# Performance work log

Measured on AMD Instinct MI355X. Metric: run time of the kernel, lower is better.

## Reference

```python
import jax, jax.numpy as jnp
import numpy as np

K_NEIGHBORS = 32  # n_neighbors, eval mode -> displacement = 0


def setup_inputs() -> dict:
    key = jax.random.key(0)
    ks = jax.random.split(key, 9)
    B, N, F = 1024, 200000, 64
    C, H = 16, 128
    return {
        "x": jax.random.normal(ks[0], (B, F), jnp.float32),
        "X_data": jax.random.normal(ks[1], (N, F), jnp.float32),
        "y": jax.random.uniform(ks[2], (N,), jnp.float32),
        "W_gate": jax.random.normal(ks[3], (F + 1, C), jnp.float32) / np.sqrt(F + 1),
        "b_gate": jax.random.normal(ks[4], (C,), jnp.float32) * 0.01,
        "W1": jax.random.normal(ks[5], (C + F, H), jnp.float32) / np.sqrt(C + F),
        "b1": jax.random.normal(ks[6], (H,), jnp.float32) * 0.01,
        "W_last": jax.random.normal(ks[7], (H, 1), jnp.float32) / np.sqrt(H),
        "b_last": jax.random.normal(ks[8], (1,), jnp.float32) * 0.01,
    }


def reference(x, X_data, y, W_gate, b_gate, W1, b1, W_last, b_last):
    # Euclidean (p=2) cdist via the expanded form: ||a-b||^2 = ||a||^2 + ||b||^2 - 2 a.b
    d2 = (jnp.sum(x * x, axis=1, keepdims=True)
          + jnp.sum(X_data * X_data, axis=1)[None, :]
          - 2.0 * (x @ X_data.T))                      # [B, N]
    dist = jnp.sqrt(jnp.maximum(d2, 0.0))
    # torch.argsort(distances,1)[:, :k] == indices of k smallest distances
    _, idx = jax.lax.top_k(-dist, K_NEIGHBORS)          # [B, K]
    neighbors = X_data[idx]                             # [B, K, F] gather
    neighbors_y = y[idx][..., None]                     # [B, K, 1]
    nf = jnp.concatenate([neighbors, neighbors_y], axis=2)  # [B, K, F+1]
    gated = jnp.tanh(nf @ W_gate + b_gate)              # [B, K, C]
    agg = jnp.sum(gated, axis=1)                        # [B, C]
    o = jnp.concatenate([x, agg], axis=1)               # [B, F+C]
    o = jnp.tanh(o @ W1 + b1)                           # activation_function = tanh
    o = jax.nn.sigmoid(o @ W_last + b_last)             # [B, 1]
    return o
```

## Files before the change

kernel.cpp:

```cpp
#include <hip/hip_runtime.h>
#include <cstdint>

#define FDIM 64
#define KNN 32
#define NBUCKET 256
#define MAXCAP 2048
#define SEG 10
#define OCAP 512

typedef unsigned int u32;
typedef unsigned long long u64;
typedef __attribute__((ext_vector_type(8))) short bf16x8;
typedef __attribute__((ext_vector_type(4))) float f32x4;

__device__ __forceinline__ float load_query(const float* __restrict__ x, int q, float4* xv) {
    const float4* xp = (const float4*)(x + (size_t)q * FDIM);
    float n0 = 0.f, n1 = 0.f, n2 = 0.f, n3 = 0.f;
#pragma unroll
    for (int k = 0; k < 16; ++k) {
        float4 v = xp[k];
        xv[k] = v;
        n0 = fmaf(v.x, v.x, n0); n1 = fmaf(v.y, v.y, n1);
        n2 = fmaf(v.z, v.z, n2); n3 = fmaf(v.w, v.w, n3);
    }
    return (n0 + n1) + (n2 + n3);
}

__device__ __forceinline__ float dot_row(const float4* __restrict__ xv, const float* __restrict__ row) {
    const float4* rv = (const float4*)row;
    float d0 = 0.f, d1 = 0.f, d2 = 0.f, d3 = 0.f;
#pragma unroll
    for (int k = 0; k < 16; ++k) {
        float4 r = rv[k];
        float4 a = xv[k];
        d0 = fmaf(a.x, r.x, d0); d1 = fmaf(a.y, r.y, d1);
        d2 = fmaf(a.z, r.z, d2); d3 = fmaf(a.w, r.w, d3);
    }
    return (d0 + d1) + (d2 + d3);
}

__global__ __launch_bounds__(256) void k_xnorm(const float* __restrict__ X, float* __restrict__ Xn, int N) {
    int i = blockIdx.x * 256 + threadIdx.x;
    if (i >= N) return;
    const float4* r = (const float4*)(X + (size_t)i * FDIM);
    float d0 = 0.f, d1 = 0.f, d2 = 0.f, d3 = 0.f;
#pragma unroll
    for (int k = 0; k < 16; ++k) {
        float4 v = r[k];
        d0 = fmaf(v.x, v.x, d0); d1 = fmaf(v.y, v.y, d1);
        d2 = fmaf(v.z, v.z, d2); d3 = fmaf(v.w, v.w, d3);
    }
    Xn[i] = (d0 + d1) + (d2 + d3);
}

__global__ __launch_bounds__(256) void k_cvtT(const float* __restrict__ src, uint4* __restrict__ dst, int n_u4) {
    int i = blockIdx.x * 256 + threadIdx.x;
    if (i >= n_u4) return;
    int lane = i & 63;
    int kk = (i >> 6) & 1;
    int g = i >> 7;
    int row = g * 16 + (lane & 15);
    int col = kk * 32 + (lane >> 4) * 8;
    const float4* s = (const float4*)(src + (size_t)row * FDIM + col);
    float4 a = s[0], b = s[1];
    ushort o[8];
    const float* f = &a.x;
#pragma unroll
    for (int k = 0; k < 4; ++k) {
        u32 u = __float_as_uint(f[k]);
        o[k] = (ushort)((u + 0x7fffu + ((u >> 16) & 1u)) >> 16);
    }
    const float* gg = &b.x;
#pragma unroll
    for (int k = 0; k < 4; ++k) {
        u32 u = __float_as_uint(gg[k]);
        o[4 + k] = (ushort)((u + 0x7fffu + ((u >> 16) & 1u)) >> 16);
    }
    dst[i] = *(uint4*)o;
}

__global__ __launch_bounds__(256) void k_hist(const float* __restrict__ x, const float* __restrict__ X,
                                              const float* __restrict__ Xn, u32* __restrict__ hist,
                                              int N, int nsamp, int sj) {
    __shared__ unsigned char h8[NBUCKET * 256];
    int t = threadIdx.x;
    u32* h32 = (u32*)h8;
#pragma unroll
    for (int k = 0; k < 64; ++k) h32[k * 256 + t] = 0;
    __syncthreads();
    int q = blockIdx.x * 256 + t;
    float4 xv[16];
    float xn = load_query(x, q, xv);
    for (int j = 0; j < sj; ++j) {
        int s = blockIdx.y * sj + j;
        int p = s * 16;
        if (s < nsamp && p < N) {
            float dp = dot_row(xv, X + (size_t)p * FDIM);
            float d2 = fmaxf(xn + Xn[p] - 2.f * dp, 0.f);
            int b = min(NBUCKET - 1, (int)d2);
            int idx = b * 256 + t;
            unsigned char v = h8[idx];
            h8[idx] = (v == 255u) ? v : (unsigned char)(v + 1);
        }
    }
    __syncthreads();
#pragma unroll
    for (int w = 0; w < 128; ++w) {
        u32 v0 = h8[(2 * w) * 256 + t];
        u32 v1 = h8[(2 * w + 1) * 256 + t];
        if (v0 | v1) atomicAdd(&hist[(size_t)q * 128 + w], v0 | (v1 << 16));
    }
}

__global__ __launch_bounds__(256) void k_thresh(const u32* __restrict__ hist, float* __restrict__ Tq, int B) {
    int q = blockIdx.x * 256 + threadIdx.x;
    if (q >= B) return;
    const u32* h = hist + (size_t)q * 128;
    int cum = 0;
    float T = (float)NBUCKET;
    for (int w = 0; w < 128; ++w) {
        u32 v = h[w];
        cum += (int)(v & 0xffffu);
        if (cum >= KNN) { T = (float)(2 * w + 1); break; }
        cum += (int)(v >> 16);
        if (cum >= KNN) { T = (float)(2 * w + 2); break; }
    }
    Tq[q] = T + 2.0f;
}

__global__ __launch_bounds__(256, 3) void k_sample_d2(
        const uint4* __restrict__ xT, const uint4* __restrict__ XT,
        const float* __restrict__ qn, const float* __restrict__ Xn,
        unsigned char* __restrict__ d2s, int S) {
    int t = threadIdx.x;
    int w = t >> 6, lane = t & 63;
    int G = lane >> 4, r = lane & 15;
    int qg = blockIdx.x;
    int wq = qg * 128 + w * 32;
    int pb = blockIdx.y * 128;

    bf16x8 afr[2][2];
#pragma unroll
    for (int kk = 0; kk < 2; ++kk)
#pragma unroll
        for (int mi = 0; mi < 2; ++mi) {
            uint4 v = xT[(size_t)(((wq >> 4) + mi) * 2 + kk) * 64 + lane];
            afr[kk][mi] = *(bf16x8*)&v;
        }
    float qr[8];
#pragma unroll
    for (int e = 0; e < 8; ++e)
        qr[e] = qn[wq + (e >> 2) * 16 + G * 4 + (e & 3)];

#pragma unroll
    for (int half = 0; half < 2; ++half) {
        int nb = half * 4;
        bf16x8 bfr[4][2];
#pragma unroll
        for (int j = 0; j < 4; ++j) {
            int gp = (pb >> 4) + nb + j;
#pragma unroll
            for (int kk = 0; kk < 2; ++kk) {
                uint4 v = XT[(size_t)(gp * 2 + kk) * 64 + lane];
                bfr[j][kk] = *(bf16x8*)&v;
            }
        }
        float xnv[4];
#pragma unroll
        for (int j = 0; j < 4; ++j) xnv[j] = Xn[pb + (nb + j) * 16 + r];

        f32x4 acc[2][4];
#pragma unroll
        for (int mi = 0; mi < 2; ++mi)
#pragma unroll
            for (int j = 0; j < 4; ++j) acc[mi][j] = (f32x4){0.f, 0.f, 0.f, 0.f};
#pragma unroll
        for (int kk = 0; kk < 2; ++kk)
#pragma unroll
            for (int j = 0; j < 4; ++j) {
                acc[0][j] = __builtin_amdgcn_mfma_f32_16x16x32_bf16(afr[kk][0], bfr[j][kk], acc[0][j], 0, 0, 0);
                acc[1][j] = __builtin_amdgcn_mfma_f32_16x16x32_bf16(afr[kk][1], bfr[j][kk], acc[1][j], 0, 0, 0);
            }
#pragma unroll
        for (int j = 0; j < 4; ++j) {
            int p = pb + (nb + j) * 16 + r;
            float xnp = xnv[j];
#pragma unroll
            for (int e = 0; e < 8; ++e) {
                float d2a = qr[e] + fmaf(-2.f, acc[e >> 2][j][e & 3], xnp);
                int b = (int)d2a;
                b = b < 0 ? 0 : (b > 255 ? 255 : b);
                int q = wq + (e >> 2) * 16 + G * 4 + (e & 3);
                d2s[(size_t)q * S + p] = (unsigned char)b;
            }
        }
    }
}

__global__ __launch_bounds__(256) void k_thresh2(const unsigned char* __restrict__ d2s,
                                                 float* __restrict__ Tq, int S) {
    __shared__ u32 h[NBUCKET];
    int t = threadIdx.x;
    int q = blockIdx.x;
    h[t] = 0;
    __syncthreads();
    const u32* row = (const u32*)(d2s + (size_t)q * S);
    int n4 = S >> 2;
    for (int i = t; i < n4; i += 256) {
        u32 v = row[i];
        atomicAdd(&h[v & 255u], 1u);
        atomicAdd(&h[(v >> 8) & 255u], 1u);
        atomicAdd(&h[(v >> 16) & 255u], 1u);
        atomicAdd(&h[v >> 24], 1u);
    }
    __syncthreads();
    if (t == 0) {
        int cum = 0;
        float T = 256.0f;
        for (int b = 0; b < NBUCKET; ++b) {
            cum += (int)h[b];
            if (cum >= KNN) { T = (float)(b + 1); break; }
        }
        Tq[q] = T + 2.0f;
    }
}

__global__ __launch_bounds__(256, 3) void k_mfma_filter(
        const uint4* __restrict__ xT, const uint4* __restrict__ XT,
        const float* __restrict__ qn, const float* __restrict__ Xn,
        const float* __restrict__ Tf,
        u32* __restrict__ cnt_seg, u32* __restrict__ list_seg,
        u32* __restrict__ ocnt, u32* __restrict__ olist,
        int N, int nStripsPad, int strip) {
    __shared__ u32 ldsCnt[128];

    int t = threadIdx.x;
    int w = t >> 6, lane = t & 63;
    int G = lane >> 4, r = lane & 15;

    int bid = blockIdx.x;
    int qg = (bid >> 3) & 7;
    int sIdx = (bid & 7) | ((bid >> 6) << 3);
    int qbase = qg * 128;
    int wq = qbase + w * 32;

    if (t < 128) ldsCnt[t] = 0;
    __syncthreads();

    bf16x8 afr[2][2];
#pragma unroll
    for (int kk = 0; kk < 2; ++kk)
#pragma unroll
        for (int mi = 0; mi < 2; ++mi) {
            uint4 v = xT[(size_t)(((wq >> 4) + mi) * 2 + kk) * 64 + lane];
            afr[kk][mi] = *(bf16x8*)&v;
        }
    float Tr[8];
#pragma unroll
    for (int e = 0; e < 8; ++e) {
        int rl = wq + (e >> 2) * 16 + G * 4 + (e & 3);
        Tr[e] = Tf[rl] - qn[rl];
    }

    u32* segBase = list_seg + ((size_t)qbase * nStripsPad + (size_t)sIdx) * SEG;

    for (int s = 0; s < strip; ++s) {
        int pb = (sIdx * strip + s) * 128;
        if (pb >= N) break;

#pragma unroll
        for (int half = 0; half < 2; ++half) {
            int nb = half * 4;
            bf16x8 bfr[4][2];
#pragma unroll
            for (int j = 0; j < 4; ++j) {
                int gp = (pb >> 4) + nb + j;
#pragma unroll
                for (int kk = 0; kk < 2; ++kk) {
                    uint4 v = XT[(size_t)(gp * 2 + kk) * 64 + lane];
                    bfr[j][kk] = *(bf16x8*)&v;
                }
            }
            float xnv[4];
#pragma unroll
            for (int j = 0; j < 4; ++j) xnv[j] = Xn[pb + (nb + j) * 16 + r];

            f32x4 acc[2][4];
#pragma unroll
            for (int mi = 0; mi < 2; ++mi)
#pragma unroll
                for (int j = 0; j < 4; ++j) acc[mi][j] = (f32x4){0.f, 0.f, 0.f, 0.f};
#pragma unroll
            for (int kk = 0; kk < 2; ++kk)
#pragma unroll
                for (int j = 0; j < 4; ++j) {
                    acc[0][j] = __builtin_amdgcn_mfma_f32_16x16x32_bf16(afr[kk][0], bfr[j][kk], acc[0][j], 0, 0, 0);
                    acc[1][j] = __builtin_amdgcn_mfma_f32_16x16x32_bf16(afr[kk][1], bfr[j][kk], acc[1][j], 0, 0, 0);
                }
#pragma unroll
            for (int j = 0; j < 4; ++j) {
                int p = pb + (nb + j) * 16 + r;
                float xnp = xnv[j];
                bool c0 = fmaf(-2.f, acc[0][j][0], xnp) < Tr[0];
                bool c1 = fmaf(-2.f, acc[0][j][1], xnp) < Tr[1];
                bool c2 = fmaf(-2.f, acc[0][j][2], xnp) < Tr[2];
                bool c3 = fmaf(-2.f, acc[0][j][3], xnp) < Tr[3];
                bool c4 = fmaf(-2.f, acc[1][j][0], xnp) < Tr[4];
                bool c5 = fmaf(-2.f, acc[1][j][1], xnp) < Tr[5];
                bool c6 = fmaf(-2.f, acc[1][j][2], xnp) < Tr[6];
                bool c7 = fmaf(-2.f, acc[1][j][3], xnp) < Tr[7];
                if ((c0 | c1 | c2 | c3 | c4 | c5 | c6 | c7) && p < N) {
#pragma unroll
                    for (int e = 0; e < 8; ++e) {
                        bool ce = (e == 0) ? c0 : (e == 1) ? c1 : (e == 2) ? c2 : (e == 3) ? c3
                                : (e == 4) ? c4 : (e == 5) ? c5 : (e == 6) ? c6 : c7;
                        if (ce) {
                            int ql = w * 32 + (e >> 2) * 16 + G * 4 + (e & 3);
                            u32 slot = atomicAdd(&ldsCnt[ql], 1u);
                            if (slot < SEG) {
                                segBase[(size_t)ql * nStripsPad * SEG + slot] = (u32)p;
                            } else {
                                u32 gs = atomicAdd(&ocnt[qbase + ql], 1u);
                                if (gs < OCAP) olist[(size_t)(qbase + ql) * OCAP + gs] = (u32)p;
                            }
                        }
                    }
                }
            }
        }
    }

    __syncthreads();
    if (t < 128) cnt_seg[(size_t)(qbase + t) * nStripsPad + sIdx] = min(ldsCnt[t], (u32)SEG);
}

__global__ __launch_bounds__(256) void k_filter_scalar(const float* __restrict__ x, const float* __restrict__ X,
                                                       const float* __restrict__ Xn, const float* __restrict__ Tq,
                                                       u32* __restrict__ cnt, u32* __restrict__ list,
                                                       int N, int cap) {
    int t = threadIdx.x;
    int q = blockIdx.x * 256 + t;
    float4 xv[16];
    float xn = load_query(x, q, xv);
    float T = Tq[q];
    int base = blockIdx.y * 1024;
    int lim = min(1024, N - base);
    for (int j = 0; j < lim; ++j) {
        int p = base + j;
        float dp = dot_row(xv, X + (size_t)p * FDIM);
        float d2 = fmaxf(xn + Xn[p] - 2.f * dp, 0.f);
        if (d2 < T) {
            u32 slot = atomicAdd(&cnt[q], 1u);
            if (slot < (u32)cap) list[(size_t)q * cap + slot] = (u32)p;
        }
    }
}

__global__ __launch_bounds__(256) void k_final(const float* __restrict__ x, const float* __restrict__ X,
                                               const float* __restrict__ y, const float* __restrict__ Xn,
                                               const float* __restrict__ Wg, const float* __restrict__ bg,
                                               const float* __restrict__ W1, const float* __restrict__ b1,
                                               const float* __restrict__ Wl, const float* __restrict__ bl,
                                               const u32* __restrict__ cnt_seg, const u32* __restrict__ list_seg,
                                               const u32* __restrict__ ocnt, const u32* __restrict__ olist,
                                               const u32* __restrict__ cnt_flat, const u32* __restrict__ list_flat,
                                               float* __restrict__ out, int nStripsPad, int cap_flat, int flat,
                                               int N) {
    __shared__ u64 keys[MAXCAP];
    __shared__ u32 nsh;
    __shared__ u64 wk[4];
    __shared__ int wp[4];
    __shared__ u32 sel[KNN];
    __shared__ float gkc[KNN * 16];
    __shared__ float aggc[16];
    __shared__ float red[128];

    int t = threadIdx.x;
    int w = t >> 6, lane = t & 63;
    int q = blockIdx.x;
    int m;

    if (flat) {
        m = (int)min(cnt_flat[q], (u32)cap_flat);
        const u32* lq = list_flat + (size_t)q * cap_flat;
        for (int i = t; i < m; i += 256) keys[i] = lq[i];
    } else {
        if (t == 0) nsh = 0;
        __syncthreads();
        for (int seg = t; seg < nStripsPad; seg += 256) {
            u32 c = cnt_seg[(size_t)q * nStripsPad + seg];
            if (c) {
                u32 base = atomicAdd(&nsh, c);
                const u32* sp = list_seg + ((size_t)q * nStripsPad + seg) * SEG;
                for (u32 j = 0; j < c; ++j) {
                    u32 idx = base + j;
                    if (idx < MAXCAP) keys[idx] = sp[j];
                }
            }
        }
        __syncthreads();
        int m0 = (int)min(nsh, (u32)MAXCAP);
        int oc = (int)min(ocnt[q], (u32)OCAP);
        for (int i = t; i < oc; i += 256)
            if (m0 + i < MAXCAP) keys[m0 + i] = olist[(size_t)q * OCAP + i];
        m = min(m0 + oc, MAXCAP);
    }
    __syncthreads();

    {
        int ch = lane & 15;
        int rsub = lane >> 4;
        float4 xq4 = ((const float4*)(x + (size_t)q * FDIM))[ch];
        float xs = fmaf(xq4.x, xq4.x, fmaf(xq4.y, xq4.y, fmaf(xq4.z, xq4.z, xq4.w * xq4.w)));
        xs += __shfl_xor(xs, 1);
        xs += __shfl_xor(xs, 2);
        xs += __shfl_xor(xs, 4);
        xs += __shfl_xor(xs, 8);
        float xn = xs;
        for (int base = w * 32; base < m; base += 128) {
            int ri[8]; u32 pp[8]; bool val[8]; float4 vv[8];
#pragma unroll
            for (int u = 0; u < 8; ++u) {
                ri[u] = base + u * 4 + rsub;
                val[u] = ri[u] < m;
                pp[u] = val[u] ? (u32)keys[ri[u]] : 0u;
            }
#pragma unroll
            for (int u = 0; u < 8; ++u)
                vv[u] = ((const float4*)(X + (size_t)pp[u] * FDIM))[ch];
#pragma unroll
            for (int u = 0; u < 8; ++u) {
                float part = fmaf(xq4.x, vv[u].x, fmaf(xq4.y, vv[u].y, fmaf(xq4.z, vv[u].z, xq4.w * vv[u].w)));
                part += __shfl_xor(part, 1);
                part += __shfl_xor(part, 2);
                part += __shfl_xor(part, 4);
                part += __shfl_xor(part, 8);
                if (val[u] && ch == 0) {
                    float d2 = fmaxf(xn + Xn[pp[u]] - 2.f * part, 0.f);
                    keys[ri[u]] = ((u64)__float_as_uint(d2) << 32) | pp[u];
                }
            }
        }
    }
    __syncthreads();

    if (m <= 512) {
        if (w == 0) {
            u64 rk[8];
#pragma unroll
            for (int i = 0; i < 8; ++i) {
                int idx = lane + (i << 6);
                rk[i] = (idx < m) ? keys[idx] : ~0ull;
            }
            for (int r = 0; r < KNN; ++r) {
                u64 bk = ~0ull;
                int bs = 0;
#pragma unroll
                for (int i = 0; i < 8; ++i)
                    if (rk[i] < bk) { bk = rk[i]; bs = i; }
                int bo = lane;
#pragma unroll
                for (int off = 1; off < 64; off <<= 1) {
                    u64 ok = __shfl_xor(bk, off);
                    int oo = __shfl_xor(bo, off);
                    if (ok < bk) { bk = ok; bo = oo; }
                }
                if (lane == bo) rk[bs] = ~0ull;
                if (lane == 0) sel[r] = (u32)bk;
            }
        }
        __syncthreads();
    } else {
        for (int r = 0; r < KNN; ++r) {
            u64 bk = ~0ull;
            int bp = -1;
            for (int i = t; i < m; i += 256) {
                u64 k = keys[i];
                if (k < bk) { bk = k; bp = i; }
            }
#pragma unroll
            for (int off = 32; off > 0; off >>= 1) {
                u64 ok = __shfl_down(bk, off);
                int op = __shfl_down(bp, off);
                if (ok < bk) { bk = ok; bp = op; }
            }
            if (lane == 0) { wk[w] = bk; wp[w] = bp; }
            __syncthreads();
            if (t == 0) {
                u64 fb = wk[0];
                int fp = wp[0];
                for (int v = 1; v < 4; ++v)
                    if (wk[v] < fb) { fb = wk[v]; fp = wp[v]; }
                sel[r] = (u32)(fb & 0xffffffffu);
                if (fp >= 0) keys[fp] = ~0ull;
            }
            __syncthreads();
        }
    }

    int c = t & 15, kk = t >> 4;
#pragma unroll
    for (int rep = 0; rep < 2; ++rep) {
        int k = kk + 16 * rep;
        int nb = min((int)sel[k], N - 1);
        const float* Xr = X + (size_t)nb * FDIM;
        float acc = bg[c];
#pragma unroll
        for (int f = 0; f < FDIM; ++f) acc = fmaf(Xr[f], Wg[f * 16 + c], acc);
        acc = fmaf(y[nb], Wg[FDIM * 16 + c], acc);
        gkc[k * 16 + c] = tanhf(acc);
    }
    __syncthreads();
    if (t < 16) {
        float s = 0.f;
#pragma unroll
        for (int k = 0; k < KNN; ++k) s += gkc[k * 16 + t];
        aggc[t] = s;
    }
    __syncthreads();
    if (t < 128) {
        const float* xq = x + (size_t)q * FDIM;
        float acc = b1[t];
#pragma unroll
        for (int f = 0; f < FDIM; ++f) acc = fmaf(xq[f], W1[f * 128 + t], acc);
#pragma unroll
        for (int cc2 = 0; cc2 < 16; ++cc2) acc = fmaf(aggc[cc2], W1[(FDIM + cc2) * 128 + t], acc);
        red[t] = tanhf(acc) * Wl[t];
    }
    __syncthreads();
    for (int off = 64; off > 0; off >>= 1) {
        if (t < off) red[t] += red[t + off];
        __syncthreads();
    }
    if (t == 0) out[q] = 1.f / (1.f + expf(-(red[0] + bl[0])));
}

extern "C" void kernel_launch(void* const* d_in, const int* in_sizes, int n_in,
                              void* d_out, int out_size, void* d_ws, size_t ws_size,
                              hipStream_t stream) {
    const float* x  = (const float*)d_in[0];
    const float* X  = (const float*)d_in[1];
    const float* y  = (const float*)d_in[2];
    const float* Wg = (const float*)d_in[3];
    const float* bg = (const float*)d_in[4];
    const float* W1 = (const float*)d_in[5];
    const float* b1 = (const float*)d_in[6];
    const float* Wl = (const float*)d_in[7];
    const float* bl = (const float*)d_in[8];
    float* out = (float*)d_out;

    int B = in_sizes[0] / FDIM;
    int N = in_sizes[1] / FDIM;

    const int strip = 8;
    int nTiles = (N + 127) / 128;
    int nStrips = (nTiles + strip - 1) / strip;
    nStrips = (nStrips + 7) & ~7;
    int nStripsPad = nStrips;
    int Npad = nStrips * strip * 128;

    char* w = (char*)d_ws;
    size_t off = 0;
    auto alloc = [&](size_t bytes) { void* p = w + off; off += (bytes + 255) & ~(size_t)255; return p; };
    float* Xn  = (float*)alloc((size_t)Npad * 4);
    float* qn  = (float*)alloc((size_t)B * 4);
    u32* hist  = (u32*)alloc((size_t)B * 512);
    float* Tq  = (float*)alloc((size_t)B * 4);
    u32* cnt   = (u32*)alloc((size_t)B * 4);

    size_t xTB = (size_t)B * 128;
    size_t XTB = (size_t)(Npad / 16) * 2048;
    size_t segCntB = (size_t)B * nStripsPad * 4;
    size_t segListB = (size_t)B * nStripsPad * SEG * 4;
    size_t ocntB = (size_t)B * 4;
    size_t olistB = (size_t)B * OCAP * 4;
    size_t rem = (ws_size > off) ? ws_size - off : 0;
    bool mfma_path = rem >= xTB + XTB + segCntB + segListB + ocntB + olistB + 4096;

    uint4* xT = nullptr; uint4* XT = nullptr;
    u32 *cnt_seg = nullptr, *list_seg = nullptr, *ocnt = nullptr, *olist = nullptr;
    u32* list_flat = nullptr; unsigned char* d2s = nullptr;
    int cap_flat = 64, Stiles = 0;
    if (mfma_path) {
        xT = (uint4*)alloc(xTB);
        XT = (uint4*)alloc(XTB);
        cnt_seg  = (u32*)alloc(segCntB);
        list_seg = (u32*)alloc(segListB);
        ocnt     = (u32*)alloc(ocntB);
        olist    = (u32*)alloc(olistB);
        rem = (ws_size > off) ? ws_size - off : 0;
        size_t st = rem / ((size_t)B * 128);
        Stiles = st > 198 ? 198 : (int)st;
        int maxFull = N / 128;
        if (Stiles > maxFull) Stiles = maxFull;
        if (Stiles >= 96) d2s = (unsigned char*)alloc((size_t)Stiles * 128 * B);
        else Stiles = 0;
    } else {
        size_t c = rem / ((size_t)B * 4);
        cap_flat = c > MAXCAP ? MAXCAP : (int)c;
        if (cap_flat < 64) cap_flat = 64;
        list_flat = (u32*)alloc((size_t)B * cap_flat * 4);
    }

    k_xnorm<<<dim3((N + 255) / 256), 256, 0, stream>>>(X, Xn, N);
    k_xnorm<<<dim3((B + 255) / 256), 256, 0, stream>>>(x, qn, B);

    if (mfma_path) {
        hipMemsetAsync(ocnt, 0, ocntB, stream);
        hipMemsetAsync(Xn + N, 0, (size_t)(Npad - N) * 4, stream);
        size_t realXT = (size_t)(N / 16) * 2048;
        hipMemsetAsync((char*)XT + realXT, 0, XTB - realXT, stream);

        int nxu4 = B * 8, nXu4 = N * 8;
        k_cvtT<<<dim3((nxu4 + 255) / 256), 256, 0, stream>>>(x, xT, nxu4);
        k_cvtT<<<dim3((nXu4 + 255) / 256), 256, 0, stream>>>(X, XT, nXu4);

        if (Stiles > 0) {
            int S = Stiles * 128;
            k_sample_d2<<<dim3(8, Stiles), 256, 0, stream>>>(xT, XT, qn, Xn, d2s, S);
            k_thresh2<<<dim3(B), 256, 0, stream>>>(d2s, Tq, S);
        } else {
            hipMemsetAsync(hist, 0, (size_t)B * 512, stream);
            int nsamp = (N + 15) / 16;
            int chunks = 128;
            int sj = (nsamp + chunks - 1) / chunks;
            k_hist<<<dim3(B / 256, chunks), 256, 0, stream>>>(x, X, Xn, hist, N, nsamp, sj);
            k_thresh<<<dim3((B + 255) / 256), 256, 0, stream>>>(hist, Tq, B);
        }

        k_mfma_filter<<<dim3(8 * nStrips), 256, 0, stream>>>(
            xT, XT, qn, Xn, Tq, cnt_seg, list_seg, ocnt, olist, N, nStripsPad, strip);

        k_final<<<dim3(B), 256, 0, stream>>>(x, X, y, Xn, Wg, bg, W1, b1, Wl, bl,
                                             cnt_seg, list_seg, ocnt, olist,
                                             nullptr, nullptr, out, nStripsPad, 0, 0, N);
    } else {
        hipMemsetAsync(cnt, 0, (size_t)B * 4, stream);
        hipMemsetAsync(hist, 0, (size_t)B * 512, stream);
        int nsamp = (N + 15) / 16;
        int chunks = 128;
        int sj = (nsamp + chunks - 1) / chunks;
        k_hist<<<dim3(B / 256, chunks), 256, 0, stream>>>(x, X, Xn, hist, N, nsamp, sj);
        k_thresh<<<dim3((B + 255) / 256), 256, 0, stream>>>(hist, Tq, B);
        k_filter_scalar<<<dim3(B / 256, (N + 1023) / 1024), 256, 0, stream>>>(
            x, X, Xn, Tq, cnt, list_flat, N, cap_flat);
        k_final<<<dim3(B), 256, 0, stream>>>(x, X, y, Xn, Wg, bg, W1, b1, Wl, bl,
                                             nullptr, nullptr, nullptr, nullptr,
                                             cnt, list_flat, out, nStripsPad, cap_flat, 1, N);
    }
}
```

Measured before the change: 287.4 us.

## Split final kernel into gather, parallel rescore, and select stages

```diff
diff --git a/kernel.cpp b/kernel.cpp
--- a/kernel.cpp
+++ b/kernel.cpp
@@ -356,18 +356,89 @@
     }
 }
 
-__global__ __launch_bounds__(256) void k_final(const float* __restrict__ x, const float* __restrict__ X,
-                                               const float* __restrict__ y, const float* __restrict__ Xn,
-                                               const float* __restrict__ Wg, const float* __restrict__ bg,
-                                               const float* __restrict__ W1, const float* __restrict__ b1,
-                                               const float* __restrict__ Wl, const float* __restrict__ bl,
-                                               const u32* __restrict__ cnt_seg, const u32* __restrict__ list_seg,
-                                               const u32* __restrict__ ocnt, const u32* __restrict__ olist,
-                                               const u32* __restrict__ cnt_flat, const u32* __restrict__ list_flat,
-                                               float* __restrict__ out, int nStripsPad, int cap_flat, int flat,
-                                               int N) {
+__global__ __launch_bounds__(256) void k_gather(const u32* __restrict__ cnt_seg, const u32* __restrict__ list_seg,
+                                                const u32* __restrict__ ocnt, const u32* __restrict__ olist,
+                                                u64* __restrict__ gkeys, u32* __restrict__ gcnt,
+                                                int nStripsPad) {
+    __shared__ u32 nsh;
+    int t = threadIdx.x;
+    int q = blockIdx.x;
+    if (t == 0) nsh = 0;
+    __syncthreads();
+    u64* gq = gkeys + (size_t)q * MAXCAP;
+    for (int seg = t; seg < nStripsPad; seg += 256) {
+        u32 c = cnt_seg[(size_t)q * nStripsPad + seg];
+        if (c) {
+            u32 base = atomicAdd(&nsh, c);
+            const u32* sp = list_seg + ((size_t)q * nStripsPad + seg) * SEG;
+            for (u32 j = 0; j < c; ++j) {
+                u32 idx = base + j;
+                if (idx < MAXCAP) gq[idx] = (u64)sp[j];
+            }
+        }
+    }
+    __syncthreads();
+    u32 m0 = min(nsh, (u32)MAXCAP);
+    u32 oc = min(ocnt[q], (u32)OCAP);
+    for (u32 i = t; i < oc; i += 256)
+        if (m0 + i < MAXCAP) gq[m0 + i] = (u64)olist[(size_t)q * OCAP + i];
+    if (t == 0) gcnt[q] = min(m0 + oc, (u32)MAXCAP);
+}
+
+__global__ __launch_bounds__(256, 4) void k_rescore(const float* __restrict__ x, const float* __restrict__ X,
+                                                    const float* __restrict__ Xn,
+                                                    u64* __restrict__ gkeys, const u32* __restrict__ gcnt) {
+    int t = threadIdx.x;
+    int w = t >> 6, lane = t & 63;
+    int q = blockIdx.x;
+    int g = blockIdx.y;
+    int m = (int)gcnt[q];
+    u64* gq = gkeys + (size_t)q * MAXCAP;
+
+    int ch = lane & 15;
+    int rsub = lane >> 4;
+    float4 xq4 = ((const float4*)(x + (size_t)q * FDIM))[ch];
+    float xs = fmaf(xq4.x, xq4.x, fmaf(xq4.y, xq4.y, fmaf(xq4.z, xq4.z, xq4.w * xq4.w)));
+    xs += __shfl_xor(xs, 1);
+    xs += __shfl_xor(xs, 2);
+    xs += __shfl_xor(xs, 4);
+    xs += __shfl_xor(xs, 8);
+    float xn = xs;
+
+    for (int base = (g * 4 + w) * 32; base < m; base += 256) {
+        int ri[8]; u32 pp[8]; bool val[8]; float4 vv[8];
+#pragma unroll
+        for (int u = 0; u < 8; ++u) {
+            ri[u] = base + u * 4 + rsub;
+            val[u] = ri[u] < m;
+            pp[u] = val[u] ? (u32)gq[ri[u]] : 0u;
+        }
+#pragma unroll
+        for (int u = 0; u < 8; ++u)
+            vv[u] = ((const float4*)(X + (size_t)pp[u] * FDIM))[ch];
+#pragma unroll
+        for (int u = 0; u < 8; ++u) {
+            float part = fmaf(xq4.x, vv[u].x, fmaf(xq4.y, vv[u].y, fmaf(xq4.z, vv[u].z, xq4.w * vv[u].w)));
+            part += __shfl_xor(part, 1);
+            part += __shfl_xor(part, 2);
+            part += __shfl_xor(part, 4);
+            part += __shfl_xor(part, 8);
+            if (val[u] && ch == 0) {
+                float d2 = fmaxf(xn + Xn[pp[u]] - 2.f * part, 0.f);
+                gq[ri[u]] = ((u64)__float_as_uint(d2) << 32) | pp[u];
+            }
+        }
+    }
+}
+
+__global__ __launch_bounds__(256) void k_select_nn(const float* __restrict__ x, const float* __restrict__ X,
+                                                   const float* __restrict__ y,
+                                                   const float* __restrict__ Wg, const float* __restrict__ bg,
+                                                   const float* __restrict__ W1, const float* __restrict__ b1,
+                                                   const float* __restrict__ Wl, const float* __restrict__ bl,
+                                                   const u64* __restrict__ gkeys, const u32* __restrict__ gcnt,
+                                                   float* __restrict__ out, int N) {
     __shared__ u64 keys[MAXCAP];
-    __shared__ u32 nsh;
     __shared__ u64 wk[4];
     __shared__ int wp[4];
     __shared__ u32 sel[KNN];
@@ -378,70 +449,10 @@
     int t = threadIdx.x;
     int w = t >> 6, lane = t & 63;
     int q = blockIdx.x;
-    int m;
-
-    if (flat) {
-        m = (int)min(cnt_flat[q], (u32)cap_flat);
-        const u32* lq = list_flat + (size_t)q * cap_flat;
-        for (int i = t; i < m; i += 256) keys[i] = lq[i];
-    } else {
-        if (t == 0) nsh = 0;
-        __syncthreads();
-        for (int seg = t; seg < nStripsPad; seg += 256) {
-            u32 c = cnt_seg[(size_t)q * nStripsPad + seg];
-            if (c) {
-                u32 base = atomicAdd(&nsh, c);
-                const u32* sp = list_seg + ((size_t)q * nStripsPad + seg) * SEG;
-                for (u32 j = 0; j < c; ++j) {
-                    u32 idx = base + j;
-                    if (idx < MAXCAP) keys[idx] = sp[j];
-                }
-            }
-        }
-        __syncthreads();
-        int m0 = (int)min(nsh, (u32)MAXCAP);
-        int oc = (int)min(ocnt[q], (u32)OCAP);
-        for (int i = t; i < oc; i += 256)
-            if (m0 + i < MAXCAP) keys[m0 + i] = olist[(size_t)q * OCAP + i];
-        m = min(m0 + oc, MAXCAP);
-    }
-    __syncthreads();
-
-    {
-        int ch = lane & 15;
-        int rsub = lane >> 4;
-        float4 xq4 = ((const float4*)(x + (size_t)q * FDIM))[ch];
-        float xs = fmaf(xq4.x, xq4.x, fmaf(xq4.y, xq4.y, fmaf(xq4.z, xq4.z, xq4.w * xq4.w)));
-        xs += __shfl_xor(xs, 1);
-        xs += __shfl_xor(xs, 2);
-        xs += __shfl_xor(xs, 4);
-        xs += __shfl_xor(xs, 8);
-        float xn = xs;
-        for (int base = w * 32; base < m; base += 128) {
-            int ri[8]; u32 pp[8]; bool val[8]; float4 vv[8];
-#pragma unroll
-            for (int u = 0; u < 8; ++u) {
-                ri[u] = base + u * 4 + rsub;
-                val[u] = ri[u] < m;
-                pp[u] = val[u] ? (u32)keys[ri[u]] : 0u;
-            }
-#pragma unroll
-            for (int u = 0; u < 8; ++u)
-                vv[u] = ((const float4*)(X + (size_t)pp[u] * FDIM))[ch];
-#pragma unroll
-            for (int u = 0; u < 8; ++u) {
-                float part = fmaf(xq4.x, vv[u].x, fmaf(xq4.y, vv[u].y, fmaf(xq4.z, vv[u].z, xq4.w * vv[u].w)));
-                part += __shfl_xor(part, 1);
-                part += __shfl_xor(part, 2);
-                part += __shfl_xor(part, 4);
-                part += __shfl_xor(part, 8);
-                if (val[u] && ch == 0) {
-                    float d2 = fmaxf(xn + Xn[pp[u]] - 2.f * part, 0.f);
-                    keys[ri[u]] = ((u64)__float_as_uint(d2) << 32) | pp[u];
-                }
-            }
-        }
-    }
+    int m = (int)gcnt[q];
+    const u64* gq = gkeys + (size_t)q * MAXCAP;
+
+    for (int i = t; i < m; i += 256) keys[i] = gq[i];
     __syncthreads();
 
     if (m <= 512) {
@@ -496,6 +507,102 @@
             }
             __syncthreads();
         }
+    }
+
+    int c = t & 15, kk = t >> 4;
+#pragma unroll
+    for (int rep = 0; rep < 2; ++rep) {
+        int k = kk + 16 * rep;
+        int nb = min((int)sel[k], N - 1);
+        const float* Xr = X + (size_t)nb * FDIM;
+        float acc = bg[c];
+#pragma unroll
+        for (int f = 0; f < FDIM; ++f) acc = fmaf(Xr[f], Wg[f * 16 + c], acc);
+        acc = fmaf(y[nb], Wg[FDIM * 16 + c], acc);
+        gkc[k * 16 + c] = tanhf(acc);
+    }
+    __syncthreads();
+    if (t < 16) {
+        float s = 0.f;
+#pragma unroll
+        for (int k = 0; k < KNN; ++k) s += gkc[k * 16 + t];
+        aggc[t] = s;
+    }
+    __syncthreads();
+    if (t < 128) {
+        const float* xq = x + (size_t)q * FDIM;
+        float acc = b1[t];
+#pragma unroll
+        for (int f = 0; f < FDIM; ++f) acc = fmaf(xq[f], W1[f * 128 + t], acc);
+#pragma unroll
+        for (int cc2 = 0; cc2 < 16; ++cc2) acc = fmaf(aggc[cc2], W1[(FDIM + cc2) * 128 + t], acc);
+        red[t] = tanhf(acc) * Wl[t];
+    }
+    __syncthreads();
+    for (int off = 64; off > 0; off >>= 1) {
+        if (t < off) red[t] += red[t + off];
+        __syncthreads();
+    }
+    if (t == 0) out[q] = 1.f / (1.f + expf(-(red[0] + bl[0])));
+}
+
+__global__ __launch_bounds__(256) void k_final_flat(const float* __restrict__ x, const float* __restrict__ X,
+                                                    const float* __restrict__ y, const float* __restrict__ Xn,
+                                                    const float* __restrict__ Wg, const float* __restrict__ bg,
+                                                    const float* __restrict__ W1, const float* __restrict__ b1,
+                                                    const float* __restrict__ Wl, const float* __restrict__ bl,
+                                                    const u32* __restrict__ cnt_flat, const u32* __restrict__ list_flat,
+                                                    float* __restrict__ out, int cap_flat, int N) {
+    __shared__ u64 keys[MAXCAP];
+    __shared__ u64 wk[4];
+    __shared__ int wp[4];
+    __shared__ u32 sel[KNN];
+    __shared__ float gkc[KNN * 16];
+    __shared__ float aggc[16];
+    __shared__ float red[128];
+
+    int t = threadIdx.x;
+    int w = t >> 6, lane = t & 63;
+    int q = blockIdx.x;
+    int m = (int)min(cnt_flat[q], (u32)cap_flat);
+    const u32* lq = list_flat + (size_t)q * cap_flat;
+    for (int i = t; i < m; i += 256) keys[i] = lq[i];
+    __syncthreads();
+
+    float4 xv[16];
+    float xn = load_query(x, q, xv);
+    for (int i = t; i < m; i += 256) {
+        u32 p = (u32)keys[i];
+        float dp = dot_row(xv, X + (size_t)p * FDIM);
+        float d2 = fmaxf(xn + Xn[p] - 2.f * dp, 0.f);
+        keys[i] = ((u64)__float_as_uint(d2) << 32) | p;
+    }
+    __syncthreads();
+
+    for (int r = 0; r < KNN; ++r) {
+        u64 bk = ~0ull;
+        int bp = -1;
+        for (int i = t; i < m; i += 256) {
+            u64 k = keys[i];
+            if (k < bk) { bk = k; bp = i; }
+        }
+#pragma unroll
+        for (int off = 32; off > 0; off >>= 1) {
+            u64 ok = __shfl_down(bk, off);
+            int op = __shfl_down(bp, off);
+            if (ok < bk) { bk = ok; bp = op; }
+        }
+        if (lane == 0) { wk[w] = bk; wp[w] = bp; }
+        __syncthreads();
+        if (t == 0) {
+            u64 fb = wk[0];
+            int fp = wp[0];
+            for (int v = 1; v < 4; ++v)
+                if (wk[v] < fb) { fb = wk[v]; fp = wp[v]; }
+            sel[r] = (u32)(fb & 0xffffffffu);
+            if (fp >= 0) keys[fp] = ~0ull;
+        }
+        __syncthreads();
     }
 
     int c = t & 15, kk = t >> 4;
@@ -574,11 +681,14 @@
     size_t segListB = (size_t)B * nStripsPad * SEG * 4;
     size_t ocntB = (size_t)B * 4;
     size_t olistB = (size_t)B * OCAP * 4;
+    size_t gkeysB = (size_t)B * MAXCAP * 8;
+    size_t gcntB = (size_t)B * 4;
     size_t rem = (ws_size > off) ? ws_size - off : 0;
-    bool mfma_path = rem >= xTB + XTB + segCntB + segListB + ocntB + olistB + 4096;
+    bool mfma_path = rem >= xTB + XTB + segCntB + segListB + ocntB + olistB + gkeysB + gcntB + 4096;
 
     uint4* xT = nullptr; uint4* XT = nullptr;
     u32 *cnt_seg = nullptr, *list_seg = nullptr, *ocnt = nullptr, *olist = nullptr;
+    u64* gkeys = nullptr; u32* gcnt = nullptr;
     u32* list_flat = nullptr; unsigned char* d2s = nullptr;
     int cap_flat = 64, Stiles = 0;
     if (mfma_path) {
@@ -588,6 +698,8 @@
         list_seg = (u32*)alloc(segListB);
         ocnt     = (u32*)alloc(ocntB);
         olist    = (u32*)alloc(olistB);
+        gkeys    = (u64*)alloc(gkeysB);
+        gcnt     = (u32*)alloc(gcntB);
         rem = (ws_size > off) ? ws_size - off : 0;
         size_t st = rem / ((size_t)B * 128);
         Stiles = st > 198 ? 198 : (int)st;
@@ -631,9 +743,10 @@
         k_mfma_filter<<<dim3(8 * nStrips), 256, 0, stream>>>(
             xT, XT, qn, Xn, Tq, cnt_seg, list_seg, ocnt, olist, N, nStripsPad, strip);
 
-        k_final<<<dim3(B), 256, 0, stream>>>(x, X, y, Xn, Wg, bg, W1, b1, Wl, bl,
-                                             cnt_seg, list_seg, ocnt, olist,
-                                             nullptr, nullptr, out, nStripsPad, 0, 0, N);
+        k_gather<<<dim3(B), 256, 0, stream>>>(cnt_seg, list_seg, ocnt, olist, gkeys, gcnt, nStripsPad);
+        k_rescore<<<dim3(B, 2), 256, 0, stream>>>(x, X, Xn, gkeys, gcnt);
+        k_select_nn<<<dim3(B), 256, 0, stream>>>(x, X, y, Wg, bg, W1, b1, Wl, bl,
+                                                 gkeys, gcnt, out, N);
     } else {
         hipMemsetAsync(cnt, 0, (size_t)B * 4, stream);
         hipMemsetAsync(hist, 0, (size_t)B * 512, stream);
@@ -644,8 +757,7 @@
         k_thresh<<<dim3((B + 255) / 256), 256, 0, stream>>>(hist, Tq, B);
         k_filter_scalar<<<dim3(B / 256, (N + 1023) / 1024), 256, 0, stream>>>(
             x, X, Xn, Tq, cnt, list_flat, N, cap_flat);
-        k_final<<<dim3(B), 256, 0, stream>>>(x, X, y, Xn, Wg, bg, W1, b1, Wl, bl,
-                                             nullptr, nullptr, nullptr, nullptr,
-                                             cnt, list_flat, out, nStripsPad, cap_flat, 1, N);
-    }
-}
+        k_final_flat<<<dim3(B), 256, 0, stream>>>(x, X, y, Xn, Wg, bg, W1, b1, Wl, bl,
+                                                  cnt, list_flat, out, cap_flat, N);
+    }
+}
```

Result: slower. 296.8 us (+3.3%).
